# Optimization experiments

Hardware: AMD Instinct MI355X
Metric: run time of the kernel (lower is better)

The kernel has to match this reference:

```python
import jax, jax.numpy as jnp
import numpy as np

N = 100000          # nodes
E = 1600000         # edges per adjacency (avg degree 16)
DIMS = [256, 128, 64]
ALPHA = 0.8
WD = 1e-4


def setup_inputs() -> dict:
    key = jax.random.key(0)
    ks = jax.random.split(key, 11)
    X = jax.random.normal(ks[0], (N, DIMS[0]), jnp.float32)
    rows = jax.random.randint(ks[1], (E,), 0, N, jnp.int32)
    cols = jax.random.randint(ks[2], (E,), 0, N, jnp.int32)
    prune_rows = jax.random.randint(ks[3], (E,), 0, N, jnp.int32)
    prune_cols = jax.random.randint(ks[4], (E,), 0, N, jnp.int32)
    # learned params (torch.randn init, scaled 0.1 for fp32 numeric headroom)
    W0 = jax.random.normal(ks[5], (DIMS[0], DIMS[1]), jnp.float32) * 0.1
    W1 = jax.random.normal(ks[6], (DIMS[1], DIMS[2]), jnp.float32) * 0.1
    v00 = jax.random.normal(ks[7], (DIMS[1], 1), jnp.float32) * 0.1
    v01 = jax.random.normal(ks[8], (DIMS[1], 1), jnp.float32) * 0.1
    pv00 = jax.random.normal(ks[9], (DIMS[1], 1), jnp.float32) * 0.1
    pv01 = jax.random.normal(ks[10], (DIMS[1], 1), jnp.float32) * 0.1
    return {"X": X, "W0": W0, "W1": W1, "v00": v00, "v01": v01,
            "pv00": pv00, "pv01": pv01, "rows": rows, "cols": cols,
            "prune_rows": prune_rows, "prune_cols": prune_cols}


def _edge_softmax(rows, logits, n):
    # row-wise softmax over sparse edge logits
    m = jax.ops.segment_max(logits, rows, num_segments=n)
    e = jnp.exp(logits - m[rows])
    s = jax.ops.segment_sum(e, rows, num_segments=n)
    return e / s[rows]


def _attention(rows, cols, H, va, vb, n):
    # logit_e = (H @ va)[src_e] + (H @ vb)[dst_e]  (binary adjacency values)
    f1 = (H @ va)[:, 0]
    f2 = (H @ vb)[:, 0]
    return _edge_softmax(rows, f1[rows] + f2[cols], n)


def _spmm(rows, cols, vals, H, n):
    # out[i] = sum_{e: rows[e]==i} vals[e] * H[cols[e]]
    return jax.ops.segment_sum(vals[:, None] * H[cols], rows, num_segments=n)


def reference(X, W0, W1, v00, v01, pv00, pv01, rows, cols, prune_rows, prune_cols):
    n = X.shape[0]
    # ---- encoder ----
    H1 = X @ W0                                   # layer 0 projection
    c = _attention(rows, cols, H1, v00, v01, n)   # C[0]
    pc = _attention(prune_rows, prune_cols, H1, pv00, pv01, n)  # prune_C[0]
    H1a = (1.0 - ALPHA) * _spmm(rows, cols, c, H1, n) \
        + ALPHA * _spmm(prune_rows, prune_cols, pc, H1, n)
    H1a = jax.nn.elu(H1a)                         # nonlinear, layer 0 != last
    H_enc = H1a @ W1                              # layer 1 == last: no attention
    # ---- decoder ----
    D = H_enc @ W1.T                              # layer 1
    D = (1.0 - ALPHA) * _spmm(rows, cols, c, D, n) \
        + ALPHA * _spmm(prune_rows, prune_cols, pc, D, n)
    D = jax.nn.elu(D)                             # nonlinear, layer 1 != 0
    X_ = D @ W0.T                                 # layer 0: plain matmul
    # ---- loss ----
    loss = jnp.sqrt(jnp.sum((X - X_) ** 2)) \
         + WD * (jnp.sum(W0 ** 2) + jnp.sum(W1 ** 2))
    return (loss, H_enc, X_)
```

## Files before the change

### kernel.cpp

```cpp
#include <hip/hip_runtime.h>
#include <math.h>

#define N_NODES 100000
#define N_EDGES 1600000
#define TOT (2 * N_NODES)
#define SCAN_NB 256
#define SCAN_CH 4

static inline int cdiv(long a, long b) { return (int)((a + b - 1) / b); }

typedef unsigned int uint;
typedef unsigned short ushort;
typedef __attribute__((ext_vector_type(8))) short short8v;
typedef __attribute__((ext_vector_type(4))) float f32x4;

__device__ inline float bf2f(uint u) { return __uint_as_float(u << 16); }
__device__ inline ushort f2bf(float f) {
    uint u = __float_as_uint(f);
    uint r = ((u >> 16) & 1u) + 0x7fffu;
    return (ushort)((u + r) >> 16);
}

template <int K, int M, bool AF32, int OUT, bool ELU, bool LOSS, bool ATTN>
__global__ __launch_bounds__(256) void gemm_mfma(const void* __restrict__ Av,
                                                 const ushort* __restrict__ Bcm,
                                                 void* __restrict__ Cv,
                                                 void* __restrict__ Cv2,
                                                 const float* __restrict__ Xref,
                                                 float* __restrict__ partial,
                                                 const float* __restrict__ va,
                                                 const float* __restrict__ vb,
                                                 const float* __restrict__ pva,
                                                 const float* __restrict__ pvb,
                                                 float* __restrict__ f1,
                                                 float* __restrict__ f2,
                                                 float* __restrict__ pf1,
                                                 float* __restrict__ pf2,
                                                 int nrows) {
    constexpr int BM = 128;
    constexpr int KP = K + 8;
    constexpr int NCT = M / 16;
    __shared__ ushort Blds[M * KP];
    __shared__ ushort Alds[BM * 32];
    const int w = threadIdx.x >> 6;
    const int l = threadIdx.x & 63;
    const int rowg = l & 15;
    const int kg = l >> 4;
    const int rbase = blockIdx.x * BM;
    {
        const uint4* src = reinterpret_cast<const uint4*>(Bcm);
        uint4* dst = reinterpret_cast<uint4*>(Blds);
        const int total = M * KP / 8;
        for (int i = threadIdx.x; i < total; i += 256) dst[i] = src[i];
    }
    f32x4 acc[2][NCT] = {};
    for (int k0 = 0; k0 < K; k0 += 32) {
        __syncthreads();
        int r = threadIdx.x >> 1;
        int kk = (threadIdx.x & 1) * 16;
        int rg = min(rbase + r, nrows - 1);
        if (AF32) {
            const float* A = (const float*)Av;
            const float4* src = reinterpret_cast<const float4*>(A + (size_t)rg * K + k0 + kk);
            ushort* dst = &Alds[r * 32 + kk];
#pragma unroll
            for (int q = 0; q < 4; ++q) {
                float4 v = src[q];
                dst[4 * q + 0] = f2bf(v.x); dst[4 * q + 1] = f2bf(v.y);
                dst[4 * q + 2] = f2bf(v.z); dst[4 * q + 3] = f2bf(v.w);
            }
        } else {
            const ushort* A = (const ushort*)Av;
            const uint4* src = reinterpret_cast<const uint4*>(A + (size_t)rg * K + k0 + kk);
            uint4* dst = reinterpret_cast<uint4*>(&Alds[r * 32 + kk]);
            dst[0] = src[0];
            dst[1] = src[1];
        }
        __syncthreads();
#pragma unroll
        for (int rt = 0; rt < 2; ++rt) {
            short8v af = *reinterpret_cast<const short8v*>(
                &Alds[(w * 32 + rt * 16 + rowg) * 32 + kg * 8]);
#pragma unroll
            for (int ct = 0; ct < NCT; ++ct) {
                short8v bf = *reinterpret_cast<const short8v*>(
                    &Blds[(ct * 16 + rowg) * KP + k0 + kg * 8]);
                acc[rt][ct] = __builtin_amdgcn_mfma_f32_16x16x32_bf16(
                    af, bf, acc[rt][ct], 0, 0, 0);
            }
        }
    }
    float lsum = 0.f;
#pragma unroll
    for (int rt = 0; rt < 2; ++rt) {
#pragma unroll
        for (int q = 0; q < 4; ++q) {
            int r = rbase + w * 32 + rt * 16 + kg * 4 + q;
            if (r >= nrows) continue;
#pragma unroll
            for (int ct = 0; ct < NCT; ++ct) {
                float o = acc[rt][ct][q];
                if (ELU) o = o > 0.f ? o : expm1f(o);
                int col = ct * 16 + rowg;
                if (OUT == 0 || OUT == 3) ((float*)Cv)[(size_t)r * M + col] = o;
                if (OUT == 2) ((ushort*)Cv)[(size_t)r * M + col] = f2bf(o);
                if (OUT == 3) ((ushort*)Cv2)[(size_t)r * M + col] = f2bf(o);
                if (LOSS) {
                    float d = o - Xref[(size_t)r * 256 + col];
                    lsum += d * d;
                }
            }
        }
    }
    if (ATTN) {
        float var[NCT], vbr[NCT], pvar[NCT], pvbr[NCT];
#pragma unroll
        for (int ct = 0; ct < NCT; ++ct) {
            int col = ct * 16 + rowg;
            var[ct] = va[col]; vbr[ct] = vb[col];
            pvar[ct] = pva[col]; pvbr[ct] = pvb[col];
        }
#pragma unroll
        for (int rt = 0; rt < 2; ++rt) {
#pragma unroll
            for (int q = 0; q < 4; ++q) {
                int r = rbase + w * 32 + rt * 16 + kg * 4 + q;
                float da = 0.f, db = 0.f, dpa = 0.f, dpb = 0.f;
#pragma unroll
                for (int ct = 0; ct < NCT; ++ct) {
                    float o = acc[rt][ct][q];
                    da += o * var[ct]; db += o * vbr[ct];
                    dpa += o * pvar[ct]; dpb += o * pvbr[ct];
                }
#pragma unroll
                for (int m = 1; m < 16; m <<= 1) {
                    da += __shfl_xor(da, m); db += __shfl_xor(db, m);
                    dpa += __shfl_xor(dpa, m); dpb += __shfl_xor(dpb, m);
                }
                if (rowg == 0 && r < nrows) {
                    f1[r] = da; f2[r] = db; pf1[r] = dpa; pf2[r] = dpb;
                }
            }
        }
    }
    if (LOSS) {
        __shared__ float smRed[4];
#pragma unroll
        for (int off = 32; off > 0; off >>= 1) lsum += __shfl_down(lsum, off);
        __syncthreads();
        if (l == 0) smRed[w] = lsum;
        __syncthreads();
        if (threadIdx.x == 0)
            partial[blockIdx.x] = smRed[0] + smRed[1] + smRed[2] + smRed[3];
    }
}

__global__ __launch_bounds__(256) void prep_all_kernel(const float* __restrict__ W0,
                                                       const float* __restrict__ W1,
                                                       ushort* __restrict__ B1,
                                                       ushort* __restrict__ B5,
                                                       ushort* __restrict__ B7,
                                                       ushort* __restrict__ B8) {
    int i = blockIdx.x * 256 + threadIdx.x;
    if (i < 32768) {
        int k = i / 128, m = i - k * 128;
        B1[m * 264 + k] = f2bf(W0[i]);
    } else if (i < 65536) {
        int j = i - 32768;
        int m = j / 128, k = j - m * 128;
        B8[m * 136 + k] = f2bf(W0[j]);
    } else if (i < 73728) {
        int j = i - 65536;
        int k = j / 64, m = j - k * 64;
        B5[m * 136 + k] = f2bf(W1[j]);
    } else if (i < 81920) {
        int j = i - 73728;
        int m = j / 64, k = j - m * 64;
        B7[m * 72 + k] = f2bf(W1[j]);
    }
}

__global__ __launch_bounds__(256) void hist2_kernel(const int* __restrict__ rows,
                                                    const int* __restrict__ prows,
                                                    int* __restrict__ deg) {
    int e = blockIdx.x * 256 + threadIdx.x;
    if (e >= 2 * N_EDGES) return;
    int b = e < N_EDGES ? rows[e] * 2 : prows[e - N_EDGES] * 2 + 1;
    atomicAdd(&deg[b], 1);
}

__device__ inline int pad8(int d) { return (d + 7) & ~7; }

__global__ __launch_bounds__(256) void scan1_kernel(const int* __restrict__ deg,
                                                    int* __restrict__ bsum) {
    __shared__ int sm[256];
    int base = (blockIdx.x * 256 + threadIdx.x) * SCAN_CH;
    int s = 0;
#pragma unroll
    for (int i = 0; i < SCAN_CH; ++i) {
        int idx = base + i;
        if (idx < TOT) s += pad8(deg[idx]);
    }
    sm[threadIdx.x] = s;
    __syncthreads();
    for (int off = 128; off > 0; off >>= 1) {
        if (threadIdx.x < off) sm[threadIdx.x] += sm[threadIdx.x + off];
        __syncthreads();
    }
    if (threadIdx.x == 0) bsum[blockIdx.x] = sm[0];
}

__global__ __launch_bounds__(256) void scan3_kernel(const int* __restrict__ deg,
                                                    const int* __restrict__ bsum,
                                                    int* __restrict__ rp) {
    __shared__ int sm[256];
    __shared__ int base0;
    if (threadIdx.x == 0) {
        int run = 0;
        for (int i = 0; i < blockIdx.x; ++i) run += bsum[i];
        base0 = run;
    }
    int base = (blockIdx.x * 256 + threadIdx.x) * SCAN_CH;
    int s = 0;
#pragma unroll
    for (int i = 0; i < SCAN_CH; ++i) {
        int idx = base + i;
        if (idx < TOT) s += pad8(deg[idx]);
    }
    sm[threadIdx.x] = s;
    __syncthreads();
    if (threadIdx.x == 0) {
        int run = base0;
        for (int t = 0; t < 256; ++t) { int tmp = sm[t]; sm[t] = run; run += tmp; }
    }
    __syncthreads();
    int off = sm[threadIdx.x];
#pragma unroll
    for (int i = 0; i < SCAN_CH; ++i) {
        int idx = base + i;
        if (idx < TOT) { rp[idx] = off; off += pad8(deg[idx]); }
        else if (idx == TOT) rp[idx] = off;
    }
}

__global__ __launch_bounds__(256) void scatter_kernel(const int* __restrict__ rlist,
                                                      const int* __restrict__ clist,
                                                      int adj,
                                                      const int* __restrict__ rp,
                                                      int* __restrict__ cur,
                                                      int* __restrict__ ccol) {
    int e = blockIdx.x * 256 + threadIdx.x;
    if (e >= N_EDGES) return;
    int b = rlist[e] * 2 + adj;
    int pos = rp[b] + atomicAdd(&cur[b], 1);
    ccol[pos] = clist[e];
}

__global__ __launch_bounds__(256) void edgeval_kernel(const int* __restrict__ rp,
                                                      const int* __restrict__ deg,
                                                      const int* __restrict__ ccol,
                                                      const float* __restrict__ f1,
                                                      const float* __restrict__ f2,
                                                      const float* __restrict__ pf1,
                                                      const float* __restrict__ pf2,
                                                      int2* __restrict__ eg) {
    int b = blockIdx.x * 16 + (threadIdx.x >> 4);
    int sl = threadIdx.x & 15;
    int adj = b & 1, r = b >> 1;
    float f1r = adj ? pf1[r] : f1[r];
    const float* f2t = adj ? pf2 : f2;
    float scale = adj ? 0.8f : 0.2f;
    int j0 = rp[b];
    int realend = j0 + deg[b];
    int pend = rp[b + 1];
    float s = 0.f;
    for (int j = j0 + sl; j < realend; j += 16)
        s += __expf(f1r + f2t[ccol[j]]);
#pragma unroll
    for (int off = 8; off > 0; off >>= 1) s += __shfl_xor(s, off);
    float inv = s > 0.f ? scale / s : 0.f;
    for (int j = j0 + sl; j < pend; j += 16) {
        if (j < realend) {
            int c = ccol[j];
            float wv = __expf(f1r + f2t[c]) * inv;
            eg[j] = make_int2(c, __float_as_int(wv));
        } else {
            eg[j] = make_int2(0, 0);
        }
    }
}

#define SPU 8
__global__ __launch_bounds__(256) void spmm_fused_kernel(const int* __restrict__ rp,
                                                         const int2* __restrict__ eg,
                                                         const ushort* __restrict__ Hb,
                                                         uint* __restrict__ outh) {
    int r = blockIdx.x * 4 + (threadIdx.x >> 6);
    int lane = threadIdx.x & 63;
    const uint* Hu = reinterpret_cast<const uint*>(Hb);
    float a0 = 0.f, a1 = 0.f;
    int j = rp[2 * r], E = rp[2 * r + 2];
    if (j < E) {
        int2 d[SPU]; uint h[SPU];
#pragma unroll
        for (int u = 0; u < SPU; ++u) d[u] = eg[j + u];
#pragma unroll
        for (int u = 0; u < SPU; ++u) h[u] = Hu[(uint)d[u].x * 64u + lane];
        j += SPU;
        for (; j < E; j += SPU) {
            int2 dn[SPU]; uint hn[SPU];
#pragma unroll
            for (int u = 0; u < SPU; ++u) dn[u] = eg[j + u];
#pragma unroll
            for (int u = 0; u < SPU; ++u) hn[u] = Hu[(uint)dn[u].x * 64u + lane];
#pragma unroll
            for (int u = 0; u < SPU; ++u) {
                float v = __int_as_float(d[u].y);
                a0 += v * bf2f(h[u] & 0xffffu);
                a1 += v * bf2f(h[u] >> 16);
            }
#pragma unroll
            for (int u = 0; u < SPU; ++u) { d[u] = dn[u]; h[u] = hn[u]; }
        }
#pragma unroll
        for (int u = 0; u < SPU; ++u) {
            float v = __int_as_float(d[u].y);
            a0 += v * bf2f(h[u] & 0xffffu);
            a1 += v * bf2f(h[u] >> 16);
        }
    }
    float o0 = a0 > 0.f ? a0 : expm1f(a0);
    float o1 = a1 > 0.f ? a1 : expm1f(a1);
    outh[(size_t)r * 64 + lane] = (uint)f2bf(o0) | ((uint)f2bf(o1) << 16);
}

__global__ __launch_bounds__(256) void spmm64_fused_kernel(const int* __restrict__ rp,
                                                           const int2* __restrict__ eg,
                                                           const ushort* __restrict__ Hb,
                                                           ushort* __restrict__ Sh) {
    int r = blockIdx.x * 4 + (threadIdx.x >> 6);
    int lane = threadIdx.x & 63;
    float a = 0.f;
    int j = rp[2 * r], E = rp[2 * r + 2];
    if (j < E) {
        int2 d[SPU]; ushort h[SPU];
#pragma unroll
        for (int u = 0; u < SPU; ++u) d[u] = eg[j + u];
#pragma unroll
        for (int u = 0; u < SPU; ++u) h[u] = Hb[(uint)d[u].x * 64u + lane];
        j += SPU;
        for (; j < E; j += SPU) {
            int2 dn[SPU]; ushort hn[SPU];
#pragma unroll
            for (int u = 0; u < SPU; ++u) dn[u] = eg[j + u];
#pragma unroll
            for (int u = 0; u < SPU; ++u) hn[u] = Hb[(uint)dn[u].x * 64u + lane];
#pragma unroll
            for (int u = 0; u < SPU; ++u)
                a += __int_as_float(d[u].y) * bf2f((uint)h[u]);
#pragma unroll
            for (int u = 0; u < SPU; ++u) { d[u] = dn[u]; h[u] = hn[u]; }
        }
#pragma unroll
        for (int u = 0; u < SPU; ++u)
            a += __int_as_float(d[u].y) * bf2f((uint)h[u]);
    }
    Sh[(size_t)r * 64 + lane] = f2bf(a);
}

__global__ __launch_bounds__(256) void sqw_reduce_kernel(const float* __restrict__ W0,
                                                         const float* __restrict__ W1,
                                                         float* __restrict__ acc) {
    __shared__ float sm[4];
    float s = 0.f;
    for (int i = blockIdx.x * 256 + threadIdx.x; i < 40960; i += gridDim.x * 256) {
        float d = i < 32768 ? W0[i] : W1[i - 32768];
        s += d * d;
    }
#pragma unroll
    for (int off = 32; off > 0; off >>= 1) s += __shfl_down(s, off);
    int lane = threadIdx.x & 63, w = threadIdx.x >> 6;
    if (lane == 0) sm[w] = s;
    __syncthreads();
    if (threadIdx.x == 0) atomicAdd(acc, sm[0] + sm[1] + sm[2] + sm[3]);
}

__global__ __launch_bounds__(256) void partial_reduce_kernel(const float* __restrict__ p,
                                                             int n, float* __restrict__ acc) {
    __shared__ float sm[4];
    float s = 0.f;
    for (int i = threadIdx.x; i < n; i += 256) s += p[i];
#pragma unroll
    for (int off = 32; off > 0; off >>= 1) s += __shfl_down(s, off);
    int lane = threadIdx.x & 63, w = threadIdx.x >> 6;
    if (lane == 0) sm[w] = s;
    __syncthreads();
    if (threadIdx.x == 0) atomicAdd(acc, sm[0] + sm[1] + sm[2] + sm[3]);
}

__global__ void finalize_kernel(const float* __restrict__ acc, float* __restrict__ out) {
    out[0] = sqrtf(acc[0]) + 1e-4f * acc[1];
}

extern "C" void kernel_launch(void* const* d_in, const int* in_sizes, int n_in,
                              void* d_out, int out_size, void* d_ws, size_t ws_size,
                              hipStream_t stream) {
    const float* X    = (const float*)d_in[0];
    const float* W0   = (const float*)d_in[1];
    const float* W1   = (const float*)d_in[2];
    const float* v00  = (const float*)d_in[3];
    const float* v01  = (const float*)d_in[4];
    const float* pv00 = (const float*)d_in[5];
    const float* pv01 = (const float*)d_in[6];
    const int* rows   = (const int*)d_in[7];
    const int* cols   = (const int*)d_in[8];
    const int* prows  = (const int*)d_in[9];
    const int* pcols  = (const int*)d_in[10];

    float* out  = (float*)d_out;
    float* Henc = out + 1;
    float* Xrec = out + 1 + (size_t)N_NODES * 64;

    ushort* bufAh  = (ushort*)(out + 6400004);
    ushort* Sh     = (ushort*)(out + 6400004);
    int*    ccol   = (int*)(out + 12800004);
    int2*   eg     = (int2*)(out + 17600004);
    ushort* HencB  = (ushort*)(out + 27200004);
    int*    deg    = (int*)(out + 28800004);
    int*    cur    = deg + TOT;

    float* ws   = (float*)d_ws;
    ushort* bufBh = (ushort*)ws;
    float* f1   = ws + (size_t)N_NODES * 128;
    float* f2   = f1 + N_NODES;
    float* pf1  = f2 + N_NODES;
    float* pf2  = pf1 + N_NODES;
    float* acc  = pf2 + N_NODES;
    ushort* B1cm = (ushort*)(acc + 4);
    ushort* B5cm = B1cm + 128 * 264;
    ushort* B7cm = B5cm + 64 * 136;
    ushort* B8cm = B7cm + 128 * 72;
    int*   rp   = (int*)(B8cm + 256 * 136);
    int*   bsum = rp + TOT + 1;
    float* partial = (float*)(bsum + SCAN_NB);

    const int n = N_NODES;
    const int EG = cdiv(N_EDGES, 256);
    const int EG2 = cdiv(2 * (long)N_EDGES, 256);

    prep_all_kernel<<<cdiv(81920, 256), 256, 0, stream>>>(W0, W1, B1cm, B5cm, B7cm, B8cm);

    gemm_mfma<256, 128, true, 2, false, false, true><<<cdiv(n, 128), 256, 0, stream>>>(
        X, B1cm, bufAh, nullptr, nullptr, nullptr,
        v00, v01, pv00, pv01, f1, f2, pf1, pf2, n);

    hipMemsetAsync(deg, 0, 2 * (size_t)TOT * sizeof(int), stream);
    hipMemsetAsync(acc, 0, 4 * sizeof(float), stream);

    hist2_kernel<<<EG2, 256, 0, stream>>>(rows, prows, deg);
    scan1_kernel<<<SCAN_NB, 256, 0, stream>>>(deg, bsum);
    scan3_kernel<<<SCAN_NB, 256, 0, stream>>>(deg, bsum, rp);
    scatter_kernel<<<EG, 256, 0, stream>>>(rows, cols, 0, rp, cur, ccol);
    scatter_kernel<<<EG, 256, 0, stream>>>(prows, pcols, 1, rp, cur, ccol);
    edgeval_kernel<<<cdiv(TOT, 16), 256, 0, stream>>>(rp, deg, ccol,
                                                      f1, f2, pf1, pf2, eg);

    spmm_fused_kernel<<<n / 4, 256, 0, stream>>>(rp, eg, bufAh, (uint*)bufBh);

    gemm_mfma<128, 64, false, 3, false, false, false><<<cdiv(n, 128), 256, 0, stream>>>(
        bufBh, B5cm, Henc, HencB, nullptr, nullptr,
        nullptr, nullptr, nullptr, nullptr, nullptr, nullptr, nullptr, nullptr, n);

    spmm64_fused_kernel<<<n / 4, 256, 0, stream>>>(rp, eg, HencB, Sh);

    gemm_mfma<64, 128, false, 2, true, false, false><<<cdiv(n, 128), 256, 0, stream>>>(
        Sh, B7cm, bufBh, nullptr, nullptr, nullptr,
        nullptr, nullptr, nullptr, nullptr, nullptr, nullptr, nullptr, nullptr, n);

    gemm_mfma<128, 256, false, 0, false, true, false><<<cdiv(n, 128), 256, 0, stream>>>(
        bufBh, B8cm, Xrec, nullptr, X, partial,
        nullptr, nullptr, nullptr, nullptr, nullptr, nullptr, nullptr, nullptr, n);

    partial_reduce_kernel<<<1, 256, 0, stream>>>(partial, cdiv(n, 128), acc + 0);
    sqw_reduce_kernel<<<20, 256, 0, stream>>>(W0, W1, acc + 1);
    finalize_kernel<<<1, 1, 0, stream>>>(acc, out);
}
```

Measured before the change: 745.4 us.

## Fuse small W1 GEMMs into encoder and decoder SpMM kernels

The 128->64 and 64->128 W1 projections are folded into the two SpMM kernels. Each block converts W1 to bf16 in LDS, stages each row's aggregated result in shared memory, and does a per-row scalar dot product. This removes two MFMA GEMM launches and their intermediate round trips through global memory. In exchange, every one of the 25000 blocks reloads and converts all of W1 (8192 elements) into LDS, and the matmul moves from MFMA to scalar FMAs.

```diff
diff --git a/kernel.cpp b/kernel.cpp
--- a/kernel.cpp
+++ b/kernel.cpp
@@ -156,10 +156,7 @@
 }
 
 __global__ __launch_bounds__(256) void prep_all_kernel(const float* __restrict__ W0,
-                                                       const float* __restrict__ W1,
                                                        ushort* __restrict__ B1,
-                                                       ushort* __restrict__ B5,
-                                                       ushort* __restrict__ B7,
                                                        ushort* __restrict__ B8) {
     int i = blockIdx.x * 256 + threadIdx.x;
     if (i < 32768) {
@@ -169,14 +166,6 @@
         int j = i - 32768;
         int m = j / 128, k = j - m * 128;
         B8[m * 136 + k] = f2bf(W0[j]);
-    } else if (i < 73728) {
-        int j = i - 65536;
-        int k = j / 64, m = j - k * 64;
-        B5[m * 136 + k] = f2bf(W1[j]);
-    } else if (i < 81920) {
-        int j = i - 73728;
-        int m = j / 64, k = j - m * 64;
-        B7[m * 72 + k] = f2bf(W1[j]);
     }
 }
 
@@ -291,11 +280,21 @@
 }
 
 #define SPU 8
-__global__ __launch_bounds__(256) void spmm_fused_kernel(const int* __restrict__ rp,
-                                                         const int2* __restrict__ eg,
-                                                         const ushort* __restrict__ Hb,
-                                                         uint* __restrict__ outh) {
+__global__ __launch_bounds__(256) void spmm_enc_kernel(const int* __restrict__ rp,
+                                                       const int2* __restrict__ eg,
+                                                       const ushort* __restrict__ Hb,
+                                                       const float* __restrict__ W1,
+                                                       float* __restrict__ Henc,
+                                                       ushort* __restrict__ HencB) {
+    __shared__ ushort W1lds[128 * 72];
+    __shared__ float sRow[4][128];
+    for (int i = threadIdx.x; i < 8192; i += 256) {
+        int k = i >> 6, m = i & 63;
+        W1lds[k * 72 + m] = f2bf(W1[i]);
+    }
+    __syncthreads();
     int r = blockIdx.x * 4 + (threadIdx.x >> 6);
+    int wid = threadIdx.x >> 6;
     int lane = threadIdx.x & 63;
     const uint* Hu = reinterpret_cast<const uint*>(Hb);
     float a0 = 0.f, a1 = 0.f;
@@ -329,16 +328,34 @@
             a1 += v * bf2f(h[u] >> 16);
         }
     }
-    float o0 = a0 > 0.f ? a0 : expm1f(a0);
-    float o1 = a1 > 0.f ? a1 : expm1f(a1);
-    outh[(size_t)r * 64 + lane] = (uint)f2bf(o0) | ((uint)f2bf(o1) << 16);
-}
-
-__global__ __launch_bounds__(256) void spmm64_fused_kernel(const int* __restrict__ rp,
-                                                           const int2* __restrict__ eg,
-                                                           const ushort* __restrict__ Hb,
-                                                           ushort* __restrict__ Sh) {
+    a0 = a0 > 0.f ? a0 : expm1f(a0);
+    a1 = a1 > 0.f ? a1 : expm1f(a1);
+    sRow[wid][2 * lane] = a0;
+    sRow[wid][2 * lane + 1] = a1;
+    asm volatile("s_waitcnt lgkmcnt(0)" ::: "memory");
+    __builtin_amdgcn_sched_barrier(0);
+    float acc = 0.f;
+#pragma unroll 8
+    for (int k = 0; k < 128; ++k)
+        acc += sRow[wid][k] * bf2f((uint)W1lds[k * 72 + lane]);
+    Henc[(size_t)r * 64 + lane] = acc;
+    HencB[(size_t)r * 64 + lane] = f2bf(acc);
+}
+
+__global__ __launch_bounds__(256) void spmm_dec_kernel(const int* __restrict__ rp,
+                                                       const int2* __restrict__ eg,
+                                                       const ushort* __restrict__ Hb,
+                                                       const float* __restrict__ W1,
+                                                       uint* __restrict__ Dh) {
+    __shared__ ushort WTlds[64 * 136];
+    __shared__ float sRow[4][64];
+    for (int i = threadIdx.x; i < 8192; i += 256) {
+        int k = i >> 7, m = i & 127;
+        WTlds[k * 136 + m] = f2bf(W1[m * 64 + k]);
+    }
+    __syncthreads();
     int r = blockIdx.x * 4 + (threadIdx.x >> 6);
+    int wid = threadIdx.x >> 6;
     int lane = threadIdx.x & 63;
     float a = 0.f;
     int j = rp[2 * r], E = rp[2 * r + 2];
@@ -365,7 +382,20 @@
         for (int u = 0; u < SPU; ++u)
             a += __int_as_float(d[u].y) * bf2f((uint)h[u]);
     }
-    Sh[(size_t)r * 64 + lane] = f2bf(a);
+    sRow[wid][lane] = a;
+    asm volatile("s_waitcnt lgkmcnt(0)" ::: "memory");
+    __builtin_amdgcn_sched_barrier(0);
+    float d0 = 0.f, d1 = 0.f;
+#pragma unroll 8
+    for (int k = 0; k < 64; ++k) {
+        float sv = sRow[wid][k];
+        uint wv = *reinterpret_cast<const uint*>(&WTlds[k * 136 + 2 * lane]);
+        d0 += sv * bf2f(wv & 0xffffu);
+        d1 += sv * bf2f(wv >> 16);
+    }
+    d0 = d0 > 0.f ? d0 : expm1f(d0);
+    d1 = d1 > 0.f ? d1 : expm1f(d1);
+    Dh[(size_t)r * 64 + lane] = (uint)f2bf(d0) | ((uint)f2bf(d1) << 16);
 }
 
 __global__ __launch_bounds__(256) void sqw_reduce_kernel(const float* __restrict__ W0,
@@ -422,7 +452,6 @@
     float* Xrec = out + 1 + (size_t)N_NODES * 64;
 
     ushort* bufAh  = (ushort*)(out + 6400004);
-    ushort* Sh     = (ushort*)(out + 6400004);
     int*    ccol   = (int*)(out + 12800004);
     int2*   eg     = (int2*)(out + 17600004);
     ushort* HencB  = (ushort*)(out + 27200004);
@@ -437,9 +466,7 @@
     float* pf2  = pf1 + N_NODES;
     float* acc  = pf2 + N_NODES;
     ushort* B1cm = (ushort*)(acc + 4);
-    ushort* B5cm = B1cm + 128 * 264;
-    ushort* B7cm = B5cm + 64 * 136;
-    ushort* B8cm = B7cm + 128 * 72;
+    ushort* B8cm = B1cm + 128 * 264;
     int*   rp   = (int*)(B8cm + 256 * 136);
     int*   bsum = rp + TOT + 1;
     float* partial = (float*)(bsum + SCAN_NB);
@@ -448,7 +475,7 @@
     const int EG = cdiv(N_EDGES, 256);
     const int EG2 = cdiv(2 * (long)N_EDGES, 256);
 
-    prep_all_kernel<<<cdiv(81920, 256), 256, 0, stream>>>(W0, W1, B1cm, B5cm, B7cm, B8cm);
+    prep_all_kernel<<<cdiv(65536, 256), 256, 0, stream>>>(W0, B1cm, B8cm);
 
     gemm_mfma<256, 128, true, 2, false, false, true><<<cdiv(n, 128), 256, 0, stream>>>(
         X, B1cm, bufAh, nullptr, nullptr, nullptr,
@@ -465,17 +492,9 @@
     edgeval_kernel<<<cdiv(TOT, 16), 256, 0, stream>>>(rp, deg, ccol,
                                                       f1, f2, pf1, pf2, eg);
 
-    spmm_fused_kernel<<<n / 4, 256, 0, stream>>>(rp, eg, bufAh, (uint*)bufBh);
-
-    gemm_mfma<128, 64, false, 3, false, false, false><<<cdiv(n, 128), 256, 0, stream>>>(
-        bufBh, B5cm, Henc, HencB, nullptr, nullptr,
-        nullptr, nullptr, nullptr, nullptr, nullptr, nullptr, nullptr, nullptr, n);
-
-    spmm64_fused_kernel<<<n / 4, 256, 0, stream>>>(rp, eg, HencB, Sh);
-
-    gemm_mfma<64, 128, false, 2, true, false, false><<<cdiv(n, 128), 256, 0, stream>>>(
-        Sh, B7cm, bufBh, nullptr, nullptr, nullptr,
-        nullptr, nullptr, nullptr, nullptr, nullptr, nullptr, nullptr, nullptr, n);
+    spmm_enc_kernel<<<n / 4, 256, 0, stream>>>(rp, eg, bufAh, W1, Henc, HencB);
+
+    spmm_dec_kernel<<<n / 4, 256, 0, stream>>>(rp, eg, HencB, W1, (uint*)bufBh);
 
     gemm_mfma<128, 256, false, 0, false, true, false><<<cdiv(n, 128), 256, 0, stream>>>(
         bufBh, B8cm, Xrec, nullptr, X, partial,
```

Result: slower. 1.061 ms (+42.3%).
